# Kernel optimization log

Hardware: AMD Instinct MI355X
Metric: run time of the kernel (lower is better)

The kernel has to match this reference:

```python
import jax, jax.numpy as jnp
import numpy as np

G, S, P = 128, 32, 16          # graphs, subgraphs per graph, nodes per subgraph
D, C, NH, OUT = 768, 256, 4, 7 # input dim, hidden dim, GAT heads, classes


def setup_inputs() -> dict:
    key = jax.random.key(0)
    ks = jax.random.split(key, 17)
    n = lambda k, shape, s=0.05: jax.random.normal(k, shape, dtype=jnp.float32) * s
    return {
        "x": jax.random.normal(ks[0], (G, S, P, D), dtype=jnp.float32),
        # GATConv(768 -> 256, heads=4, concat=False): lin weight, att vectors, bias
        "gat_W": n(ks[1], (D, NH * C)),
        "att_src": n(ks[2], (NH, C)),
        "att_dst": n(ks[3], (NH, C)),
        "gat_b": n(ks[4], (C,)),
        # GRU(256 -> 256), torch layout [3*H, in]
        "gru_Wih": n(ks[5], (3 * C, C)),
        "gru_Whh": n(ks[6], (3 * C, C)),
        "gru_bih": n(ks[7], (3 * C,)),
        "gru_bhh": n(ks[8], (3 * C,)),
        # scale_up_projection Linear(256 -> 768)
        "up_W": n(ks[9], (D, C)),
        "up_b": n(ks[10], (D,)),
        # speaker_projection Linear(1536 -> 768) + ReLU
        "sp_W": n(ks[11], (D, 2 * D)),
        "sp_b": n(ks[12], (D,)),
        # GlobalAttention gate Linear(256 -> 1)
        "att_W": n(ks[13], (1, C)),
        "att_b": n(ks[14], (1,)),
        # classifier Linear(256 -> 7)
        "cls_W": n(ks[15], (OUT, C)),
        "cls_b": n(ks[16], (OUT,)),
    }


def _gat(x, W, a_src, a_dst, b):
    # PyG GATConv on a star graph (speaker = local node 0 -> all others) with
    # default add_self_loops=True, negative_slope=0.2, concat=False (mean over heads).
    # x: [G, P, D]
    h = jnp.einsum('gpd,dhc->gphc', x, W.reshape(D, NH, C))     # per-head transform
    es = jnp.sum(h * a_src, -1)                                 # [G, P, NH]
    ed = jnp.sum(h * a_dst, -1)
    lrelu = lambda v: jnp.where(v > 0, v, 0.2 * v)
    e_spk = lrelu(es[:, :1] + ed)   # edge speaker -> t
    e_slf = lrelu(es + ed)          # self loop t -> t
    w = jax.nn.softmax(jnp.stack([e_spk, e_slf], -1), axis=-1)  # [G, P, NH, 2]
    # for t == 0 both terms are h[:,0] and weights sum to 1, matching the
    # speaker node receiving only its self loop.
    out = w[..., 0:1] * h[:, :1] + w[..., 1:2] * h              # [G, P, NH, C]
    return out.mean(axis=2) + b


def _gru_cell(xin, h, Wih, Whh, bih, bhh):
    gi = xin @ Wih.T + bih
    gh = h @ Whh.T + bhh
    ir, iz, inn = jnp.split(gi, 3, -1)
    hr, hz, hn = jnp.split(gh, 3, -1)
    r = jax.nn.sigmoid(ir + hr)
    z = jax.nn.sigmoid(iz + hz)
    return (1 - z) * jnp.tanh(inn + r * hn) + z * h


def _forward(x, gat_W, att_src, att_dst, gat_b, gru_Wih, gru_Whh, gru_bih, gru_bhh,
             up_W, up_b, sp_W, sp_b, att_W, att_b, cls_W, cls_b):
    g, s, p, d = x.shape
    m0 = _gat(x[:, 0], gat_W, att_src, att_dst, gat_b)  # [G, P, C]
    h0 = jnp.zeros((g, p, C), x.dtype)

    def step(carry, _):
        h_run, m_prev = carry
        # running GRU hidden over memory prefix, then one zero-input step
        # (equivalent to rerunning the GRU over [m_0..m_{j-1}, 0])
        h_run = _gru_cell(m_prev, h_run, gru_Wih, gru_Whh, gru_bih, gru_bhh)
        h_nxt = _gru_cell(jnp.zeros_like(h_run), h_run, gru_Wih, gru_Whh, gru_bih, gru_bhh)
        pooled = h_nxt @ up_W.T + up_b                  # [G, P, D]
        # faithful to source: non_speaker_indices covers ALL nodes (torch.equal
        # shape-mismatch bug), and speaker_info is read AFTER the overwrite,
        # so the speaker concat is [pooled, pooled] and raw x[:, j>=1] is unused.
        spk = jnp.concatenate([pooled[:, 0], pooled[:, 0]], -1)  # [G, 2D]
        spk = jax.nn.relu(spk @ sp_W.T + sp_b)
        x_new = pooled.at[:, 0].set(spk)
        m = _gat(x_new, gat_W, att_src, att_dst, gat_b)
        return (h_run, m), m

    (_, _), ms = jax.lax.scan(step, (h0, m0), None, length=s - 1)
    mem = jnp.concatenate([m0[None], ms], axis=0)        # [S, G, P, C]
    # GlobalAttention pool over the P nodes of each subgraph memory state
    gate = jax.nn.softmax(jnp.squeeze(mem @ att_W.T + att_b, -1), axis=-1)  # [S, G, P]
    pooled = jnp.einsum('sgp,sgpc->sgc', gate, mem)
    logits = pooled @ cls_W.T + cls_b                    # [S, G, OUT]
    # torch stacks graph-major: [G*S, 1, OUT]
    return jnp.transpose(logits, (1, 0, 2)).reshape(g * s, 1, OUT)


def reference(x, gat_W, att_src, att_dst, gat_b, gru_Wih, gru_Whh, gru_bih, gru_bhh,
              up_W, up_b, sp_W, sp_b, att_W, att_b, cls_W, cls_b):
    return _forward(x, gat_W, att_src, att_dst, gat_b, gru_Wih, gru_Whh, gru_bih,
                    gru_bhh, up_W, up_b, sp_W, sp_b, att_W, att_b, cls_W, cls_b)
```

## Files before the change

kernel.cpp:

```cpp
#include <hip/hip_runtime.h>
#include <math.h>

#define NG 128
#define NS 32
#define NP 16
#define ND 768
#define NC 256
#define NHD 4
#define NOUT 7
#define NR 2048

typedef unsigned short ushortT;
typedef short bf16x8 __attribute__((ext_vector_type(8)));
typedef float f32x4 __attribute__((ext_vector_type(4)));

__device__ __forceinline__ ushortT f2b(float f) {
    union { float f; unsigned u; } v; v.f = f;
    unsigned r = (v.u + 0x7FFF + ((v.u >> 16) & 1)) >> 16;
    return (ushortT)r;
}
__device__ __forceinline__ float sigf(float v) { return 1.f / (1.f + expf(-v)); }

#define MFMA16(a, b, c) __builtin_amdgcn_mfma_f32_16x16x32_bf16((a), (b), (c), 0, 0, 0)

__global__ __launch_bounds__(256) void bgemm_kernel(
    const ushortT* __restrict__ A, const ushortT* __restrict__ Bt,
    const float* __restrict__ bias, float* __restrict__ outF,
    ushortT* __restrict__ outH, int N, int K, int act, int rowStride)
{
    __shared__ short As[64 * 40];
    __shared__ short Bs[64 * 40];
    const int tid = threadIdx.x;
    const int lane = tid & 63, wid = tid >> 6;
    const int quad = lane >> 4, l15 = lane & 15;
    const int row0 = blockIdx.y * 64, col0 = blockIdx.x * 64;
    const int mh = (wid & 1) * 32, nh = (wid >> 1) * 32;
    const int sr = tid >> 2, skq = (tid & 3) * 8;
    const ushortT* aptr = A + (size_t)(row0 + sr) * K;
    const ushortT* bptr = Bt + (size_t)(col0 + sr) * K;

    f32x4 acc[2][2];
    for (int i = 0; i < 2; ++i)
        for (int j = 0; j < 2; ++j) acc[i][j] = (f32x4){0.f, 0.f, 0.f, 0.f};

    for (int kk = 0; kk < K; kk += 32) {
        __syncthreads();
        *(uint4*)&As[sr * 40 + skq] = *(const uint4*)(aptr + kk + skq);
        *(uint4*)&Bs[sr * 40 + skq] = *(const uint4*)(bptr + kk + skq);
        __syncthreads();
        bf16x8 af0 = *(const bf16x8*)&As[(mh + l15) * 40 + quad * 8];
        bf16x8 af1 = *(const bf16x8*)&As[(mh + 16 + l15) * 40 + quad * 8];
        bf16x8 bf0 = *(const bf16x8*)&Bs[(nh + l15) * 40 + quad * 8];
        bf16x8 bf1 = *(const bf16x8*)&Bs[(nh + 16 + l15) * 40 + quad * 8];
        acc[0][0] = MFMA16(af0, bf0, acc[0][0]);
        acc[0][1] = MFMA16(af0, bf1, acc[0][1]);
        acc[1][0] = MFMA16(af1, bf0, acc[1][0]);
        acc[1][1] = MFMA16(af1, bf1, acc[1][1]);
    }
#pragma unroll
    for (int mt = 0; mt < 2; ++mt)
#pragma unroll
        for (int nt = 0; nt < 2; ++nt) {
            const int gc = col0 + nh + nt * 16 + l15;
            const float bv = bias ? bias[gc] : 0.f;
#pragma unroll
            for (int r = 0; r < 4; ++r) {
                const int gr = (row0 + mh + mt * 16 + quad * 4 + r) * rowStride;
                float v = acc[mt][nt][r] + bv;
                if (act) v = fmaxf(v, 0.f);
                if (outF) outF[(size_t)gr * N + gc] = v;
                if (outH) outH[(size_t)gr * N + gc] = f2b(v);
            }
        }
}

__global__ __launch_bounds__(256) void gru1_mfma_kernel(
    const ushortT* __restrict__ mB, const ushortT* __restrict__ hB,
    const ushortT* __restrict__ WihB, const ushortT* __restrict__ WhhB,
    const float* __restrict__ bih, const float* __restrict__ bhh,
    float* __restrict__ hF, ushortT* __restrict__ hBout)
{
    __shared__ short As[2 * 32 * 264];
    __shared__ short Bs[384 * 40];
    const int tid = threadIdx.x;
    const int lane = tid & 63, wid = tid >> 6;
    const int quad = lane >> 4, l15 = lane & 15;
    const int row0 = blockIdx.y * 32;
    const int n0 = blockIdx.x * 64;
    const int mt = wid & 1, nhh = (wid >> 1) * 32;

    for (int c = tid; c < 2048; c += 256) {
        const int mat = c >> 10, r2 = c & 1023, row = r2 >> 5, kc = (r2 & 31) * 8;
        const ushortT* src = (mat ? hB : mB) + (size_t)(row0 + row) * NC + kc;
        *(uint4*)&As[mat * 8448 + row * 264 + kc] = *(const uint4*)src;
    }
    f32x4 acc[2][3][2];
    for (int w = 0; w < 2; ++w)
        for (int g = 0; g < 3; ++g)
            for (int n = 0; n < 2; ++n) acc[w][g][n] = (f32x4){0.f, 0.f, 0.f, 0.f};

    for (int kk = 0; kk < 256; kk += 32) {
        __syncthreads();
        for (int c = tid; c < 1536; c += 256) {
            const int j = c >> 2, kq = (c & 3) * 8;
            const int w = j / 192, j2 = j - w * 192, gt = j2 >> 6, nloc = j2 & 63;
            const ushortT* src = (w ? WhhB : WihB) +
                (size_t)(gt * 256 + n0 + nloc) * NC + kk + kq;
            *(uint4*)&Bs[j * 40 + kq] = *(const uint4*)src;
        }
        __syncthreads();
        bf16x8 af0 = *(const bf16x8*)&As[(mt * 16 + l15) * 264 + kk + quad * 8];
        bf16x8 af1 = *(const bf16x8*)&As[8448 + (mt * 16 + l15) * 264 + kk + quad * 8];
#pragma unroll
        for (int gt = 0; gt < 3; ++gt)
#pragma unroll
            for (int nt = 0; nt < 2; ++nt) {
                const int jb = gt * 64 + nhh + nt * 16 + l15;
                bf16x8 b0 = *(const bf16x8*)&Bs[jb * 40 + quad * 8];
                bf16x8 b1 = *(const bf16x8*)&Bs[(192 + jb) * 40 + quad * 8];
                acc[0][gt][nt] = MFMA16(af0, b0, acc[0][gt][nt]);
                acc[1][gt][nt] = MFMA16(af1, b1, acc[1][gt][nt]);
            }
    }
#pragma unroll
    for (int nt = 0; nt < 2; ++nt) {
        const int c = n0 + nhh + nt * 16 + l15;
        const float br = bih[c], bz = bih[256 + c], bn = bih[512 + c];
        const float cr = bhh[c], cz = bhh[256 + c], cn = bhh[512 + c];
#pragma unroll
        for (int r = 0; r < 4; ++r) {
            const int grow = row0 + mt * 16 + quad * 4 + r;
            const size_t idx = (size_t)grow * NC + c;
            const float hold = hF[idx];
            const float rg = sigf(acc[0][0][nt][r] + br + acc[1][0][nt][r] + cr);
            const float zg = sigf(acc[0][1][nt][r] + bz + acc[1][1][nt][r] + cz);
            const float ng = tanhf(acc[0][2][nt][r] + bn + rg * (acc[1][2][nt][r] + cn));
            const float hn = (1.f - zg) * ng + zg * hold;
            hF[idx] = hn;
            hBout[idx] = f2b(hn);
        }
    }
}

__global__ __launch_bounds__(256) void gru2_mfma_kernel(
    const ushortT* __restrict__ hB, const ushortT* __restrict__ WhhB,
    const float* __restrict__ bih, const float* __restrict__ bhh,
    const float* __restrict__ hF, ushortT* __restrict__ hnB,
    ushortT* __restrict__ h0c)
{
    __shared__ short As[32 * 264];
    __shared__ short Bs[192 * 40];
    const int tid = threadIdx.x;
    const int lane = tid & 63, wid = tid >> 6;
    const int quad = lane >> 4, l15 = lane & 15;
    const int row0 = blockIdx.y * 32;
    const int n0 = blockIdx.x * 64;
    const int mt = wid & 1, nhh = (wid >> 1) * 32;

    for (int c = tid; c < 1024; c += 256) {
        const int row = c >> 5, kc = (c & 31) * 8;
        *(uint4*)&As[row * 264 + kc] =
            *(const uint4*)(hB + (size_t)(row0 + row) * NC + kc);
    }
    f32x4 acc[3][2];
    for (int g = 0; g < 3; ++g)
        for (int n = 0; n < 2; ++n) acc[g][n] = (f32x4){0.f, 0.f, 0.f, 0.f};

    for (int kk = 0; kk < 256; kk += 32) {
        __syncthreads();
        for (int c = tid; c < 768; c += 256) {
            const int j = c >> 2, kq = (c & 3) * 8;
            const int gt = j >> 6, nloc = j & 63;
            *(uint4*)&Bs[j * 40 + kq] =
                *(const uint4*)(WhhB + (size_t)(gt * 256 + n0 + nloc) * NC + kk + kq);
        }
        __syncthreads();
        bf16x8 af = *(const bf16x8*)&As[(mt * 16 + l15) * 264 + kk + quad * 8];
#pragma unroll
        for (int gt = 0; gt < 3; ++gt)
#pragma unroll
            for (int nt = 0; nt < 2; ++nt) {
                const int jb = gt * 64 + nhh + nt * 16 + l15;
                bf16x8 b = *(const bf16x8*)&Bs[jb * 40 + quad * 8];
                acc[gt][nt] = MFMA16(af, b, acc[gt][nt]);
            }
    }
#pragma unroll
    for (int nt = 0; nt < 2; ++nt) {
        const int c = n0 + nhh + nt * 16 + l15;
        const float br = bih[c], bz = bih[256 + c], bn = bih[512 + c];
        const float cr = bhh[c], cz = bhh[256 + c], cn = bhh[512 + c];
#pragma unroll
        for (int r = 0; r < 4; ++r) {
            const int grow = row0 + mt * 16 + quad * 4 + r;
            const size_t idx = (size_t)grow * NC + c;
            const float rg = sigf(br + acc[0][nt][r] + cr);
            const float zg = sigf(bz + acc[1][nt][r] + cz);
            const float ng = tanhf(bn + rg * (acc[2][nt][r] + cn));
            const float hv = (1.f - zg) * ng + zg * hF[idx];
            const ushortT hb = f2b(hv);
            hnB[idx] = hb;
            if ((grow & 15) == 0) h0c[(size_t)(grow >> 4) * NC + c] = hb;
        }
    }
}

__global__ __launch_bounds__(256) void fin_kernel(
    const float* __restrict__ hbuf, const float* __restrict__ att_src,
    const float* __restrict__ att_dst, const float* __restrict__ gat_b,
    const float* __restrict__ attW, const float* __restrict__ attb,
    const float* __restrict__ clsW, const float* __restrict__ clsb,
    ushortT* __restrict__ mB, float* __restrict__ outp, int s)
{
    const int g = blockIdx.x, tid = threadIdx.x;
    const int lane = tid & 63, wid = tid >> 6;
    __shared__ float es_s[16][4], ed_s[16][4];
    __shared__ float m_s[16][260];
    __shared__ float gate_s[16];
    __shared__ float pooled_s[256];
    const float* hb = hbuf + (size_t)g * NP * (NHD * NC);

    for (int pi = 0; pi < 4; ++pi) {
        const int p = wid * 4 + pi;
        const float* row = hb + p * (NHD * NC);
        float ss[4] = {0.f, 0.f, 0.f, 0.f}, sd[4] = {0.f, 0.f, 0.f, 0.f};
#pragma unroll
        for (int i = 0; i < 16; ++i) {
            const int col = lane + 64 * i;
            const float v = row[col];
            ss[i >> 2] += v * att_src[col];
            sd[i >> 2] += v * att_dst[col];
        }
        for (int off = 32; off; off >>= 1)
#pragma unroll
            for (int h = 0; h < 4; ++h) {
                ss[h] += __shfl_down(ss[h], off);
                sd[h] += __shfl_down(sd[h], off);
            }
        if (lane == 0)
#pragma unroll
            for (int h = 0; h < 4; ++h) { es_s[p][h] = ss[h]; ed_s[p][h] = sd[h]; }
    }
    __syncthreads();
    {
        const int p = tid >> 4, cb = (tid & 15) * 16;
        float accv[16];
#pragma unroll
        for (int cj = 0; cj < 16; ++cj) accv[cj] = 0.f;
#pragma unroll
        for (int h = 0; h < 4; ++h) {
            float e1 = es_s[0][h] + ed_s[p][h]; e1 = e1 > 0.f ? e1 : 0.2f * e1;
            float e2 = es_s[p][h] + ed_s[p][h]; e2 = e2 > 0.f ? e2 : 0.2f * e2;
            const float mx = fmaxf(e1, e2);
            float w0 = expf(e1 - mx), w1 = expf(e2 - mx);
            const float inv = 1.f / (w0 + w1);
            w0 *= inv; w1 *= inv;
            const float* r0 = hb + h * NC + cb;
            const float* rp = hb + p * (NHD * NC) + h * NC + cb;
#pragma unroll
            for (int cj = 0; cj < 16; ++cj) accv[cj] += w0 * r0[cj] + w1 * rp[cj];
        }
#pragma unroll
        for (int cj = 0; cj < 16; ++cj) {
            const float v = accv[cj] * 0.25f + gat_b[cb + cj];
            m_s[p][cb + cj] = v;
            mB[(size_t)(g * NP + p) * NC + cb + cj] = f2b(v);
        }
    }
    __syncthreads();
    for (int pi = 0; pi < 4; ++pi) {
        const int p = wid * 4 + pi;
        float sg = 0.f;
#pragma unroll
        for (int i = 0; i < 4; ++i) { const int c = lane + 64 * i; sg += m_s[p][c] * attW[c]; }
        for (int off = 32; off; off >>= 1) sg += __shfl_down(sg, off);
        if (lane == 0) gate_s[p] = sg + attb[0];
    }
    __syncthreads();
    float mx = -1e30f;
#pragma unroll
    for (int p = 0; p < 16; ++p) mx = fmaxf(mx, gate_s[p]);
    float ge[16], ssum = 0.f;
#pragma unroll
    for (int p = 0; p < 16; ++p) { ge[p] = expf(gate_s[p] - mx); ssum += ge[p]; }
    const float inv = 1.f / ssum;
    {
        float pc = 0.f;
#pragma unroll
        for (int p = 0; p < 16; ++p) pc += ge[p] * m_s[p][tid];
        pooled_s[tid] = pc * inv;
    }
    __syncthreads();
    const int o = tid >> 5, l32 = tid & 31;
    if (o < NOUT) {
        float a = 0.f;
#pragma unroll
        for (int i = 0; i < 8; ++i) {
            const int c = l32 + 32 * i;
            a += pooled_s[c] * clsW[o * NC + c];
        }
        for (int off = 16; off; off >>= 1) a += __shfl_down(a, off);
        if (l32 == 0) outp[((size_t)g * NS + s) * NOUT + o] = a + clsb[o];
    }
}

__global__ __launch_bounds__(256) void cast_kernel(const float* __restrict__ a,
                                                   ushortT* __restrict__ b, int n) {
    const int i = blockIdx.x * 256 + threadIdx.x;
    if (i < n) b[i] = f2b(a[i]);
}
__global__ __launch_bounds__(256) void gatT_kernel(const float* __restrict__ gW,
                                                   ushortT* __restrict__ gB) {
    const int idx = blockIdx.x * 256 + threadIdx.x;
    const int c = idx / ND, d = idx - c * ND;
    gB[idx] = f2b(gW[(size_t)d * (NHD * NC) + c]);
}
__global__ __launch_bounds__(256) void upwT_kernel(const float* __restrict__ upW,
                                                   ushortT* __restrict__ o) {
    const int idx = blockIdx.x * 256 + threadIdx.x;
    const int k = idx / ND, d = idx - k * ND;
    o[idx] = f2b(upW[(size_t)d * NC + k]);
}
__global__ __launch_bounds__(256) void bcomb_kernel(const float* __restrict__ gW,
                                                    const float* __restrict__ up_b,
                                                    float* __restrict__ bc) {
    const int c = blockIdx.x * 256 + threadIdx.x;
    if (c >= NHD * NC) return;
    float a = 0.f;
    for (int d = 0; d < ND; ++d) a += up_b[d] * gW[(size_t)d * (NHD * NC) + c];
    bc[c] = a;
}
__global__ __launch_bounds__(256) void spwc_kernel(const float* __restrict__ spW,
                                                   float* __restrict__ o) {
    const int idx = blockIdx.x * 256 + threadIdx.x;
    const int r = idx / ND, d = idx - r * ND;
    o[idx] = spW[(size_t)r * (2 * ND) + d] + spW[(size_t)r * (2 * ND) + ND + d];
}
__global__ __launch_bounds__(256) void wus_kernel(const float* __restrict__ spWc,
                                                  const float* __restrict__ upW,
                                                  ushortT* __restrict__ WusB) {
    const int c = threadIdx.x;
    const int o0 = blockIdx.x * 16;
    float acc[16];
#pragma unroll
    for (int i = 0; i < 16; ++i) acc[i] = 0.f;
    for (int d = 0; d < ND; ++d) {
        const float u = upW[(size_t)d * NC + c];
#pragma unroll
        for (int i = 0; i < 16; ++i) acc[i] += spWc[(size_t)(o0 + i) * ND + d] * u;
    }
#pragma unroll
    for (int i = 0; i < 16; ++i) WusB[(size_t)(o0 + i) * NC + c] = f2b(acc[i]);
}
__global__ __launch_bounds__(256) void bus_kernel(const float* __restrict__ spWc,
                                                  const float* __restrict__ up_b,
                                                  const float* __restrict__ sp_b,
                                                  float* __restrict__ bus) {
    const int o = blockIdx.x * 256 + threadIdx.x;
    if (o >= ND) return;
    float a = sp_b[o];
    const float* sr = spWc + (size_t)o * ND;
    for (int d = 0; d < ND; ++d) a += sr[d] * up_b[d];
    bus[o] = a;
}
__global__ __launch_bounds__(256) void x0_kernel(const float* __restrict__ x,
                                                 ushortT* __restrict__ xb) {
    const int idx = blockIdx.x * 256 + threadIdx.x;
    const int row = idx / ND, d = idx - row * ND;
    const int g = row >> 4, p = row & 15;
    xb[idx] = f2b(x[((size_t)g * (NS * NP) + p) * ND + d]);
}
__global__ __launch_bounds__(256) void zh_kernel(float* hF, ushortT* hB) {
    const int idx = blockIdx.x * 256 + threadIdx.x;
    hF[idx] = 0.f;
    hB[idx] = 0;
}

extern "C" void kernel_launch(void* const* d_in, const int* in_sizes, int n_in,
                              void* d_out, int out_size, void* d_ws, size_t ws_size,
                              hipStream_t stream) {
    (void)in_sizes; (void)n_in; (void)out_size; (void)ws_size;
    const float* x       = (const float*)d_in[0];
    const float* gat_W   = (const float*)d_in[1];
    const float* att_src = (const float*)d_in[2];
    const float* att_dst = (const float*)d_in[3];
    const float* gat_b   = (const float*)d_in[4];
    const float* gru_Wih = (const float*)d_in[5];
    const float* gru_Whh = (const float*)d_in[6];
    const float* gru_bih = (const float*)d_in[7];
    const float* gru_bhh = (const float*)d_in[8];
    const float* up_W    = (const float*)d_in[9];
    const float* up_b    = (const float*)d_in[10];
    const float* sp_W    = (const float*)d_in[11];
    const float* sp_b    = (const float*)d_in[12];
    const float* att_W   = (const float*)d_in[13];
    const float* att_b   = (const float*)d_in[14];
    const float* cls_W   = (const float*)d_in[15];
    const float* cls_b   = (const float*)d_in[16];
    float* outp = (float*)d_out;

    char* w = (char*)d_ws;
    ushortT* xb    = (ushortT*)w; w += (size_t)NR * ND * 2;
    ushortT* WihB  = (ushortT*)w; w += (size_t)(3 * NC) * NC * 2;
    ushortT* WhhB  = (ushortT*)w; w += (size_t)(3 * NC) * NC * 2;
    ushortT* gatB  = (ushortT*)w; w += (size_t)(NHD * NC) * ND * 2;
    ushortT* WusB  = (ushortT*)w; w += (size_t)ND * NC * 2;
    ushortT* upWT  = (ushortT*)w; w += (size_t)NC * ND * 2;
    ushortT* WcombB= (ushortT*)w; w += (size_t)(NHD * NC) * NC * 2;
    float*   bcomb = (float*)w;   w += (size_t)(NHD * NC) * 4;
    float*   spWc  = (float*)w;   w += (size_t)ND * ND * 4;
    float*   bus   = (float*)w;   w += (size_t)ND * 4;
    float*   hF    = (float*)w;   w += (size_t)NR * NC * 4;
    ushortT* hB    = (ushortT*)w; w += (size_t)NR * NC * 2;
    ushortT* hnB   = (ushortT*)w; w += (size_t)NR * NC * 2;
    ushortT* h0c   = (ushortT*)w; w += (size_t)NG * NC * 2;
    ushortT* spkB  = (ushortT*)w; w += (size_t)NG * ND * 2;
    float*   hbuf  = (float*)w;   w += (size_t)NR * (NHD * NC) * 4;
    ushortT* mB    = (ushortT*)w; w += (size_t)NR * NC * 2;

    cast_kernel<<<768, 256, 0, stream>>>(gru_Wih, WihB, 3 * NC * NC);
    cast_kernel<<<768, 256, 0, stream>>>(gru_Whh, WhhB, 3 * NC * NC);
    gatT_kernel<<<(NHD * NC * ND) / 256, 256, 0, stream>>>(gat_W, gatB);
    upwT_kernel<<<(NC * ND) / 256, 256, 0, stream>>>(up_W, upWT);
    bcomb_kernel<<<(NHD * NC) / 256, 256, 0, stream>>>(gat_W, up_b, bcomb);
    spwc_kernel<<<(ND * ND) / 256, 256, 0, stream>>>(sp_W, spWc);
    wus_kernel<<<ND / 16, 256, 0, stream>>>(spWc, up_W, WusB);
    bus_kernel<<<3, 256, 0, stream>>>(spWc, up_b, sp_b, bus);
    x0_kernel<<<(NR * ND) / 256, 256, 0, stream>>>(x, xb);
    zh_kernel<<<(NR * NC) / 256, 256, 0, stream>>>(hF, hB);
    bgemm_kernel<<<dim3(NC / 64, (NHD * NC) / 64), 256, 0, stream>>>(
        gatB, upWT, nullptr, nullptr, WcombB, NC, ND, 0, 1);

    bgemm_kernel<<<dim3((NHD * NC) / 64, NR / 64), 256, 0, stream>>>(
        xb, gatB, nullptr, hbuf, nullptr, NHD * NC, ND, 0, 1);
    fin_kernel<<<NG, 256, 0, stream>>>(hbuf, att_src, att_dst, gat_b,
                                       att_W, att_b, cls_W, cls_b, mB, outp, 0);

    for (int j = 1; j < NS; ++j) {
        gru1_mfma_kernel<<<dim3(NC / 64, NR / 32), 256, 0, stream>>>(
            mB, hB, WihB, WhhB, gru_bih, gru_bhh, hF, hB);
        gru2_mfma_kernel<<<dim3(NC / 64, NR / 32), 256, 0, stream>>>(
            hB, WhhB, gru_bih, gru_bhh, hF, hnB, h0c);
        bgemm_kernel<<<dim3(ND / 64, NG / 64), 256, 0, stream>>>(
            h0c, WusB, bus, nullptr, spkB, ND, NC, 1, 1);
        bgemm_kernel<<<dim3((NHD * NC) / 64, NR / 64), 256, 0, stream>>>(
            hnB, WcombB, bcomb, hbuf, nullptr, NHD * NC, NC, 0, 1);
        bgemm_kernel<<<dim3((NHD * NC) / 64, NG / 64), 256, 0, stream>>>(
            spkB, gatB, nullptr, hbuf, nullptr, NHD * NC, ND, 0, 16);
        fin_kernel<<<NG, 256, 0, stream>>>(hbuf, att_src, att_dst, gat_b,
                                           att_W, att_b, cls_W, cls_b, mB, outp, j);
    }
}
```

Baseline: 2.630 ms.

## Fuse entire recurrent GRU/GAT time loop into one persistent per-graph kernel

Replaces the per-timestep sequence of GRU, projection, GAT GEMM and finalize kernel launches with a single kernel that runs one block per graph across all timesteps. Hidden state, GAT features and memory stay in shared memory and registers instead of round-tripping through global buffers, and the input cast and zero-init kernels are folded in. This removes launch overhead and global traffic. The cost is only 128 blocks of parallelism, and every block streams the weights from global/L2 without LDS tiling at each step.

```diff
diff --git a/kernel.cpp b/kernel.cpp
--- a/kernel.cpp
+++ b/kernel.cpp
@@ -19,14 +19,306 @@
     unsigned r = (v.u + 0x7FFF + ((v.u >> 16) & 1)) >> 16;
     return (ushortT)r;
 }
+__device__ __forceinline__ float b2f(ushortT u) {
+    union { unsigned u; float f; } v; v.u = ((unsigned)u) << 16; return v.f;
+}
 __device__ __forceinline__ float sigf(float v) { return 1.f / (1.f + expf(-v)); }
 
 #define MFMA16(a, b, c) __builtin_amdgcn_mfma_f32_16x16x32_bf16((a), (b), (c), 0, 0, 0)
+
+__global__ __launch_bounds__(512, 2) void mega_kernel(
+    const float* __restrict__ x,
+    const ushortT* __restrict__ WihB, const ushortT* __restrict__ WhhB,
+    const ushortT* __restrict__ WcombB, const float* __restrict__ bcomb,
+    const ushortT* __restrict__ gatB, const ushortT* __restrict__ WusB,
+    const float* __restrict__ busv,
+    const float* __restrict__ bih, const float* __restrict__ bhh,
+    const float* __restrict__ att_src, const float* __restrict__ att_dst,
+    const float* __restrict__ gat_b, const float* __restrict__ attW,
+    const float* __restrict__ attb, const float* __restrict__ clsW,
+    const float* __restrict__ clsb, float* __restrict__ outp)
+{
+    __shared__ float hb[16][1032];
+    __shared__ float m_f[16][264];
+    __shared__ ushortT hrun_b[16][264];
+    __shared__ ushortT hnxt_b[16][264];
+    __shared__ ushortT spk_b[800];
+    __shared__ float ats_s[1024], atd_s[1024], gatb_s[256];
+    __shared__ float es_s[16][4], ed_s[16][4], gate_s[16], pooled_s[256];
+
+    const int g = blockIdx.x, tid = threadIdx.x;
+    const int w = tid >> 6, lane = tid & 63;
+    const int quad = lane >> 4, l15 = lane & 15;
+
+    for (int i = tid; i < 1024; i += 512) { ats_s[i] = att_src[i]; atd_s[i] = att_dst[i]; }
+    for (int i = tid; i < 256; i += 512) gatb_s[i] = gat_b[i];
+    for (int i = tid; i < 16 * 264; i += 512) ((ushortT*)hrun_b)[i] = 0;
+    float hreg[2][4];
+#pragma unroll
+    for (int nt = 0; nt < 2; ++nt)
+#pragma unroll
+        for (int r = 0; r < 4; ++r) hreg[nt][r] = 0.f;
+    __syncthreads();
+
+    auto fin = [&](int s) {
+        for (int p = w; p < 16; p += 8) {
+            const float* row = hb[p];
+            float ss[4] = {0.f, 0.f, 0.f, 0.f}, sd[4] = {0.f, 0.f, 0.f, 0.f};
+#pragma unroll
+            for (int i = 0; i < 16; ++i) {
+                const int col = lane + 64 * i;
+                const float v = row[col];
+                ss[i >> 2] += v * ats_s[col];
+                sd[i >> 2] += v * atd_s[col];
+            }
+            for (int off = 32; off; off >>= 1)
+#pragma unroll
+                for (int h = 0; h < 4; ++h) {
+                    ss[h] += __shfl_down(ss[h], off);
+                    sd[h] += __shfl_down(sd[h], off);
+                }
+            if (lane == 0)
+#pragma unroll
+                for (int h = 0; h < 4; ++h) { es_s[p][h] = ss[h]; ed_s[p][h] = sd[h]; }
+        }
+        __syncthreads();
+        {
+            const int p = tid >> 5, cb = (tid & 31) * 8;
+            float accv[8];
+#pragma unroll
+            for (int cj = 0; cj < 8; ++cj) accv[cj] = 0.f;
+#pragma unroll
+            for (int h = 0; h < 4; ++h) {
+                float e1 = es_s[0][h] + ed_s[p][h]; e1 = e1 > 0.f ? e1 : 0.2f * e1;
+                float e2 = es_s[p][h] + ed_s[p][h]; e2 = e2 > 0.f ? e2 : 0.2f * e2;
+                const float mx = fmaxf(e1, e2);
+                float w0 = expf(e1 - mx), w1 = expf(e2 - mx);
+                const float inv = 1.f / (w0 + w1);
+                w0 *= inv; w1 *= inv;
+                const float* r0 = &hb[0][h * NC + cb];
+                const float* rp = &hb[p][h * NC + cb];
+#pragma unroll
+                for (int cj = 0; cj < 8; ++cj) accv[cj] += w0 * r0[cj] + w1 * rp[cj];
+            }
+#pragma unroll
+            for (int cj = 0; cj < 8; ++cj)
+                m_f[p][cb + cj] = accv[cj] * 0.25f + gatb_s[cb + cj];
+        }
+        __syncthreads();
+        for (int p = w; p < 16; p += 8) {
+            float sg = 0.f;
+#pragma unroll
+            for (int i = 0; i < 4; ++i) { const int c = lane + 64 * i; sg += m_f[p][c] * attW[c]; }
+            for (int off = 32; off; off >>= 1) sg += __shfl_down(sg, off);
+            if (lane == 0) gate_s[p] = sg + attb[0];
+        }
+        __syncthreads();
+        if (tid < 256) {
+            float mx = -1e30f;
+#pragma unroll
+            for (int p = 0; p < 16; ++p) mx = fmaxf(mx, gate_s[p]);
+            float se = 0.f, pc = 0.f;
+#pragma unroll
+            for (int p = 0; p < 16; ++p) {
+                const float e = expf(gate_s[p] - mx);
+                se += e; pc += e * m_f[p][tid];
+            }
+            pooled_s[tid] = pc / se;
+        }
+        __syncthreads();
+        if (w < NOUT) {
+            float a = 0.f;
+#pragma unroll
+            for (int i = 0; i < 4; ++i) {
+                const int c = lane + 64 * i;
+                a += pooled_s[c] * clsW[w * NC + c];
+            }
+            for (int off = 32; off; off >>= 1) a += __shfl_down(a, off);
+            if (lane == 0) outp[((size_t)g * NS + s) * NOUT + w] = a + clsb[w];
+        }
+        __syncthreads();
+    };
+
+    {
+        const float* xg = x + (size_t)g * (NS * NP * ND);
+        f32x4 a0[8];
+#pragma unroll
+        for (int t = 0; t < 8; ++t) a0[t] = (f32x4){0.f, 0.f, 0.f, 0.f};
+        for (int kk = 0; kk < ND; kk += 32) {
+            const float* ap = xg + (size_t)l15 * ND + kk + quad * 8;
+            bf16x8 af;
+#pragma unroll
+            for (int i = 0; i < 8; ++i) af[i] = (short)f2b(ap[i]);
+#pragma unroll
+            for (int t = 0; t < 8; ++t) {
+                const int col = w * 128 + t * 16 + l15;
+                bf16x8 bv = *(const bf16x8*)(gatB + (size_t)col * ND + kk + quad * 8);
+                a0[t] = MFMA16(af, bv, a0[t]);
+            }
+        }
+#pragma unroll
+        for (int t = 0; t < 8; ++t) {
+            const int col = w * 128 + t * 16 + l15;
+#pragma unroll
+            for (int r = 0; r < 4; ++r) hb[quad * 4 + r][col] = a0[t][r];
+        }
+    }
+    __syncthreads();
+    fin(0);
+
+    for (int j = 1; j < NS; ++j) {
+        {
+            f32x4 a1[2][3][2];
+#pragma unroll
+            for (int mm = 0; mm < 2; ++mm)
+#pragma unroll
+                for (int gt = 0; gt < 3; ++gt)
+#pragma unroll
+                    for (int nt = 0; nt < 2; ++nt) a1[mm][gt][nt] = (f32x4){0.f, 0.f, 0.f, 0.f};
+            for (int kk = 0; kk < NC; kk += 32) {
+                const float* mp = &m_f[l15][kk + quad * 8];
+                bf16x8 afm;
+#pragma unroll
+                for (int i = 0; i < 8; ++i) afm[i] = (short)f2b(mp[i]);
+                bf16x8 afh = *(const bf16x8*)&hrun_b[l15][kk + quad * 8];
+#pragma unroll
+                for (int gt = 0; gt < 3; ++gt)
+#pragma unroll
+                    for (int nt = 0; nt < 2; ++nt) {
+                        const int col = gt * 256 + w * 32 + nt * 16 + l15;
+                        bf16x8 b1 = *(const bf16x8*)(WihB + (size_t)col * NC + kk + quad * 8);
+                        bf16x8 b2 = *(const bf16x8*)(WhhB + (size_t)col * NC + kk + quad * 8);
+                        a1[0][gt][nt] = MFMA16(afm, b1, a1[0][gt][nt]);
+                        a1[1][gt][nt] = MFMA16(afh, b2, a1[1][gt][nt]);
+                    }
+            }
+            __syncthreads();
+#pragma unroll
+            for (int nt = 0; nt < 2; ++nt) {
+                const int c = w * 32 + nt * 16 + l15;
+                const float br = bih[c], bz = bih[256 + c], bn = bih[512 + c];
+                const float cr = bhh[c], cz = bhh[256 + c], cn = bhh[512 + c];
+#pragma unroll
+                for (int r = 0; r < 4; ++r) {
+                    const int row = quad * 4 + r;
+                    const float rg = sigf(a1[0][0][nt][r] + br + a1[1][0][nt][r] + cr);
+                    const float zg = sigf(a1[0][1][nt][r] + bz + a1[1][1][nt][r] + cz);
+                    const float ng = tanhf(a1[0][2][nt][r] + bn + rg * (a1[1][2][nt][r] + cn));
+                    const float hn = (1.f - zg) * ng + zg * hreg[nt][r];
+                    hreg[nt][r] = hn;
+                    hrun_b[row][c] = f2b(hn);
+                }
+            }
+        }
+        __syncthreads();
+
+        {
+            f32x4 a2[3][2];
+#pragma unroll
+            for (int gt = 0; gt < 3; ++gt)
+#pragma unroll
+                for (int nt = 0; nt < 2; ++nt) a2[gt][nt] = (f32x4){0.f, 0.f, 0.f, 0.f};
+            for (int kk = 0; kk < NC; kk += 32) {
+                bf16x8 afh = *(const bf16x8*)&hrun_b[l15][kk + quad * 8];
+#pragma unroll
+                for (int gt = 0; gt < 3; ++gt)
+#pragma unroll
+                    for (int nt = 0; nt < 2; ++nt) {
+                        const int col = gt * 256 + w * 32 + nt * 16 + l15;
+                        bf16x8 b2 = *(const bf16x8*)(WhhB + (size_t)col * NC + kk + quad * 8);
+                        a2[gt][nt] = MFMA16(afh, b2, a2[gt][nt]);
+                    }
+            }
+#pragma unroll
+            for (int nt = 0; nt < 2; ++nt) {
+                const int c = w * 32 + nt * 16 + l15;
+                const float br = bih[c], bz = bih[256 + c], bn = bih[512 + c];
+                const float cr = bhh[c], cz = bhh[256 + c], cn = bhh[512 + c];
+#pragma unroll
+                for (int r = 0; r < 4; ++r) {
+                    const int row = quad * 4 + r;
+                    const float rg = sigf(br + a2[0][nt][r] + cr);
+                    const float zg = sigf(bz + a2[1][nt][r] + cz);
+                    const float ng = tanhf(bn + rg * (a2[2][nt][r] + cn));
+                    const float hv = (1.f - zg) * ng + zg * hreg[nt][r];
+                    hnxt_b[row][c] = f2b(hv);
+                }
+            }
+        }
+        __syncthreads();
+
+        for (int it = 0; it < 6; ++it) {
+            const int slot = it * 512 + tid;
+            const int o = slot >> 2, part = slot & 3;
+            float s = 0.f;
+#pragma unroll
+            for (int k8 = 0; k8 < 8; ++k8) {
+                const int k = part * 64 + k8 * 8;
+                bf16x8 hv8 = *(const bf16x8*)&hnxt_b[0][k];
+                bf16x8 wv8 = *(const bf16x8*)(WusB + (size_t)o * NC + k);
+#pragma unroll
+                for (int i = 0; i < 8; ++i) s += b2f((ushortT)hv8[i]) * b2f((ushortT)wv8[i]);
+            }
+            s += __shfl_down(s, 1);
+            s += __shfl_down(s, 2);
+            if (part == 0) spk_b[o] = f2b(fmaxf(s + busv[o], 0.f));
+        }
+        __syncthreads();
+
+        {
+            f32x4 ag[8];
+#pragma unroll
+            for (int t = 0; t < 8; ++t) ag[t] = (f32x4){0.f, 0.f, 0.f, 0.f};
+            for (int kk = 0; kk < NC; kk += 32) {
+                bf16x8 af;
+                if (l15 == 0) {
+#pragma unroll
+                    for (int i = 0; i < 8; ++i) af[i] = 0;
+                } else {
+                    af = *(const bf16x8*)&hnxt_b[l15][kk + quad * 8];
+                }
+#pragma unroll
+                for (int t = 0; t < 8; ++t) {
+                    const int col = w * 128 + t * 16 + l15;
+                    bf16x8 bv = *(const bf16x8*)(WcombB + (size_t)col * NC + kk + quad * 8);
+                    ag[t] = MFMA16(af, bv, ag[t]);
+                }
+            }
+            for (int kk = 0; kk < ND; kk += 32) {
+                bf16x8 af;
+                if (l15 == 0) {
+                    af = *(const bf16x8*)&spk_b[kk + quad * 8];
+                } else {
+#pragma unroll
+                    for (int i = 0; i < 8; ++i) af[i] = 0;
+                }
+#pragma unroll
+                for (int t = 0; t < 8; ++t) {
+                    const int col = w * 128 + t * 16 + l15;
+                    bf16x8 bv = *(const bf16x8*)(gatB + (size_t)col * ND + kk + quad * 8);
+                    ag[t] = MFMA16(af, bv, ag[t]);
+                }
+            }
+#pragma unroll
+            for (int t = 0; t < 8; ++t) {
+                const int col = w * 128 + t * 16 + l15;
+                const float bc = bcomb[col];
+#pragma unroll
+                for (int r = 0; r < 4; ++r) {
+                    const int row = quad * 4 + r;
+                    hb[row][col] = ag[t][r] + (row ? bc : 0.f);
+                }
+            }
+        }
+        __syncthreads();
+
+        fin(j);
+    }
+}
 
 __global__ __launch_bounds__(256) void bgemm_kernel(
     const ushortT* __restrict__ A, const ushortT* __restrict__ Bt,
-    const float* __restrict__ bias, float* __restrict__ outF,
-    ushortT* __restrict__ outH, int N, int K, int act, int rowStride)
+    ushortT* __restrict__ outH, int N, int K)
 {
     __shared__ short As[64 * 40];
     __shared__ short Bs[64 * 40];
@@ -62,246 +354,12 @@
 #pragma unroll
         for (int nt = 0; nt < 2; ++nt) {
             const int gc = col0 + nh + nt * 16 + l15;
-            const float bv = bias ? bias[gc] : 0.f;
 #pragma unroll
             for (int r = 0; r < 4; ++r) {
-                const int gr = (row0 + mh + mt * 16 + quad * 4 + r) * rowStride;
-                float v = acc[mt][nt][r] + bv;
-                if (act) v = fmaxf(v, 0.f);
-                if (outF) outF[(size_t)gr * N + gc] = v;
-                if (outH) outH[(size_t)gr * N + gc] = f2b(v);
-            }
-        }
-}
-
-__global__ __launch_bounds__(256) void gru1_mfma_kernel(
-    const ushortT* __restrict__ mB, const ushortT* __restrict__ hB,
-    const ushortT* __restrict__ WihB, const ushortT* __restrict__ WhhB,
-    const float* __restrict__ bih, const float* __restrict__ bhh,
-    float* __restrict__ hF, ushortT* __restrict__ hBout)
-{
-    __shared__ short As[2 * 32 * 264];
-    __shared__ short Bs[384 * 40];
-    const int tid = threadIdx.x;
-    const int lane = tid & 63, wid = tid >> 6;
-    const int quad = lane >> 4, l15 = lane & 15;
-    const int row0 = blockIdx.y * 32;
-    const int n0 = blockIdx.x * 64;
-    const int mt = wid & 1, nhh = (wid >> 1) * 32;
-
-    for (int c = tid; c < 2048; c += 256) {
-        const int mat = c >> 10, r2 = c & 1023, row = r2 >> 5, kc = (r2 & 31) * 8;
-        const ushortT* src = (mat ? hB : mB) + (size_t)(row0 + row) * NC + kc;
-        *(uint4*)&As[mat * 8448 + row * 264 + kc] = *(const uint4*)src;
-    }
-    f32x4 acc[2][3][2];
-    for (int w = 0; w < 2; ++w)
-        for (int g = 0; g < 3; ++g)
-            for (int n = 0; n < 2; ++n) acc[w][g][n] = (f32x4){0.f, 0.f, 0.f, 0.f};
-
-    for (int kk = 0; kk < 256; kk += 32) {
-        __syncthreads();
-        for (int c = tid; c < 1536; c += 256) {
-            const int j = c >> 2, kq = (c & 3) * 8;
-            const int w = j / 192, j2 = j - w * 192, gt = j2 >> 6, nloc = j2 & 63;
-            const ushortT* src = (w ? WhhB : WihB) +
-                (size_t)(gt * 256 + n0 + nloc) * NC + kk + kq;
-            *(uint4*)&Bs[j * 40 + kq] = *(const uint4*)src;
-        }
-        __syncthreads();
-        bf16x8 af0 = *(const bf16x8*)&As[(mt * 16 + l15) * 264 + kk + quad * 8];
-        bf16x8 af1 = *(const bf16x8*)&As[8448 + (mt * 16 + l15) * 264 + kk + quad * 8];
-#pragma unroll
-        for (int gt = 0; gt < 3; ++gt)
-#pragma unroll
-            for (int nt = 0; nt < 2; ++nt) {
-                const int jb = gt * 64 + nhh + nt * 16 + l15;
-                bf16x8 b0 = *(const bf16x8*)&Bs[jb * 40 + quad * 8];
-                bf16x8 b1 = *(const bf16x8*)&Bs[(192 + jb) * 40 + quad * 8];
-                acc[0][gt][nt] = MFMA16(af0, b0, acc[0][gt][nt]);
-                acc[1][gt][nt] = MFMA16(af1, b1, acc[1][gt][nt]);
-            }
-    }
-#pragma unroll
-    for (int nt = 0; nt < 2; ++nt) {
-        const int c = n0 + nhh + nt * 16 + l15;
-        const float br = bih[c], bz = bih[256 + c], bn = bih[512 + c];
-        const float cr = bhh[c], cz = bhh[256 + c], cn = bhh[512 + c];
-#pragma unroll
-        for (int r = 0; r < 4; ++r) {
-            const int grow = row0 + mt * 16 + quad * 4 + r;
-            const size_t idx = (size_t)grow * NC + c;
-            const float hold = hF[idx];
-            const float rg = sigf(acc[0][0][nt][r] + br + acc[1][0][nt][r] + cr);
-            const float zg = sigf(acc[0][1][nt][r] + bz + acc[1][1][nt][r] + cz);
-            const float ng = tanhf(acc[0][2][nt][r] + bn + rg * (acc[1][2][nt][r] + cn));
-            const float hn = (1.f - zg) * ng + zg * hold;
-            hF[idx] = hn;
-            hBout[idx] = f2b(hn);
-        }
-    }
-}
-
-__global__ __launch_bounds__(256) void gru2_mfma_kernel(
-    const ushortT* __restrict__ hB, const ushortT* __restrict__ WhhB,
-    const float* __restrict__ bih, const float* __restrict__ bhh,
-    const float* __restrict__ hF, ushortT* __restrict__ hnB,
-    ushortT* __restrict__ h0c)
-{
-    __shared__ short As[32 * 264];
-    __shared__ short Bs[192 * 40];
-    const int tid = threadIdx.x;
-    const int lane = tid & 63, wid = tid >> 6;
-    const int quad = lane >> 4, l15 = lane & 15;
-    const int row0 = blockIdx.y * 32;
-    const int n0 = blockIdx.x * 64;
-    const int mt = wid & 1, nhh = (wid >> 1) * 32;
-
-    for (int c = tid; c < 1024; c += 256) {
-        const int row = c >> 5, kc = (c & 31) * 8;
-        *(uint4*)&As[row * 264 + kc] =
-            *(const uint4*)(hB + (size_t)(row0 + row) * NC + kc);
-    }
-    f32x4 acc[3][2];
-    for (int g = 0; g < 3; ++g)
-        for (int n = 0; n < 2; ++n) acc[g][n] = (f32x4){0.f, 0.f, 0.f, 0.f};
-
-    for (int kk = 0; kk < 256; kk += 32) {
-        __syncthreads();
-        for (int c = tid; c < 768; c += 256) {
-            const int j = c >> 2, kq = (c & 3) * 8;
-            const int gt = j >> 6, nloc = j & 63;
-            *(uint4*)&Bs[j * 40 + kq] =
-                *(const uint4*)(WhhB + (size_t)(gt * 256 + n0 + nloc) * NC + kk + kq);
-        }
-        __syncthreads();
-        bf16x8 af = *(const bf16x8*)&As[(mt * 16 + l15) * 264 + kk + quad * 8];
-#pragma unroll
-        for (int gt = 0; gt < 3; ++gt)
-#pragma unroll
-            for (int nt = 0; nt < 2; ++nt) {
-                const int jb = gt * 64 + nhh + nt * 16 + l15;
-                bf16x8 b = *(const bf16x8*)&Bs[jb * 40 + quad * 8];
-                acc[gt][nt] = MFMA16(af, b, acc[gt][nt]);
-            }
-    }
-#pragma unroll
-    for (int nt = 0; nt < 2; ++nt) {
-        const int c = n0 + nhh + nt * 16 + l15;
-        const float br = bih[c], bz = bih[256 + c], bn = bih[512 + c];
-        const float cr = bhh[c], cz = bhh[256 + c], cn = bhh[512 + c];
-#pragma unroll
-        for (int r = 0; r < 4; ++r) {
-            const int grow = row0 + mt * 16 + quad * 4 + r;
-            const size_t idx = (size_t)grow * NC + c;
-            const float rg = sigf(br + acc[0][nt][r] + cr);
-            const float zg = sigf(bz + acc[1][nt][r] + cz);
-            const float ng = tanhf(bn + rg * (acc[2][nt][r] + cn));
-            const float hv = (1.f - zg) * ng + zg * hF[idx];
-            const ushortT hb = f2b(hv);
-            hnB[idx] = hb;
-            if ((grow & 15) == 0) h0c[(size_t)(grow >> 4) * NC + c] = hb;
-        }
-    }
-}
-
-__global__ __launch_bounds__(256) void fin_kernel(
-    const float* __restrict__ hbuf, const float* __restrict__ att_src,
-    const float* __restrict__ att_dst, const float* __restrict__ gat_b,
-    const float* __restrict__ attW, const float* __restrict__ attb,
-    const float* __restrict__ clsW, const float* __restrict__ clsb,
-    ushortT* __restrict__ mB, float* __restrict__ outp, int s)
-{
-    const int g = blockIdx.x, tid = threadIdx.x;
-    const int lane = tid & 63, wid = tid >> 6;
-    __shared__ float es_s[16][4], ed_s[16][4];
-    __shared__ float m_s[16][260];
-    __shared__ float gate_s[16];
-    __shared__ float pooled_s[256];
-    const float* hb = hbuf + (size_t)g * NP * (NHD * NC);
-
-    for (int pi = 0; pi < 4; ++pi) {
-        const int p = wid * 4 + pi;
-        const float* row = hb + p * (NHD * NC);
-        float ss[4] = {0.f, 0.f, 0.f, 0.f}, sd[4] = {0.f, 0.f, 0.f, 0.f};
-#pragma unroll
-        for (int i = 0; i < 16; ++i) {
-            const int col = lane + 64 * i;
-            const float v = row[col];
-            ss[i >> 2] += v * att_src[col];
-            sd[i >> 2] += v * att_dst[col];
-        }
-        for (int off = 32; off; off >>= 1)
-#pragma unroll
-            for (int h = 0; h < 4; ++h) {
-                ss[h] += __shfl_down(ss[h], off);
-                sd[h] += __shfl_down(sd[h], off);
-            }
-        if (lane == 0)
-#pragma unroll
-            for (int h = 0; h < 4; ++h) { es_s[p][h] = ss[h]; ed_s[p][h] = sd[h]; }
-    }
-    __syncthreads();
-    {
-        const int p = tid >> 4, cb = (tid & 15) * 16;
-        float accv[16];
-#pragma unroll
-        for (int cj = 0; cj < 16; ++cj) accv[cj] = 0.f;
-#pragma unroll
-        for (int h = 0; h < 4; ++h) {
-            float e1 = es_s[0][h] + ed_s[p][h]; e1 = e1 > 0.f ? e1 : 0.2f * e1;
-            float e2 = es_s[p][h] + ed_s[p][h]; e2 = e2 > 0.f ? e2 : 0.2f * e2;
-            const float mx = fmaxf(e1, e2);
-            float w0 = expf(e1 - mx), w1 = expf(e2 - mx);
-            const float inv = 1.f / (w0 + w1);
-            w0 *= inv; w1 *= inv;
-            const float* r0 = hb + h * NC + cb;
-            const float* rp = hb + p * (NHD * NC) + h * NC + cb;
-#pragma unroll
-            for (int cj = 0; cj < 16; ++cj) accv[cj] += w0 * r0[cj] + w1 * rp[cj];
-        }
-#pragma unroll
-        for (int cj = 0; cj < 16; ++cj) {
-            const float v = accv[cj] * 0.25f + gat_b[cb + cj];
-            m_s[p][cb + cj] = v;
-            mB[(size_t)(g * NP + p) * NC + cb + cj] = f2b(v);
-        }
-    }
-    __syncthreads();
-    for (int pi = 0; pi < 4; ++pi) {
-        const int p = wid * 4 + pi;
-        float sg = 0.f;
-#pragma unroll
-        for (int i = 0; i < 4; ++i) { const int c = lane + 64 * i; sg += m_s[p][c] * attW[c]; }
-        for (int off = 32; off; off >>= 1) sg += __shfl_down(sg, off);
-        if (lane == 0) gate_s[p] = sg + attb[0];
-    }
-    __syncthreads();
-    float mx = -1e30f;
-#pragma unroll
-    for (int p = 0; p < 16; ++p) mx = fmaxf(mx, gate_s[p]);
-    float ge[16], ssum = 0.f;
-#pragma unroll
-    for (int p = 0; p < 16; ++p) { ge[p] = expf(gate_s[p] - mx); ssum += ge[p]; }
-    const float inv = 1.f / ssum;
-    {
-        float pc = 0.f;
-#pragma unroll
-        for (int p = 0; p < 16; ++p) pc += ge[p] * m_s[p][tid];
-        pooled_s[tid] = pc * inv;
-    }
-    __syncthreads();
-    const int o = tid >> 5, l32 = tid & 31;
-    if (o < NOUT) {
-        float a = 0.f;
-#pragma unroll
-        for (int i = 0; i < 8; ++i) {
-            const int c = l32 + 32 * i;
-            a += pooled_s[c] * clsW[o * NC + c];
-        }
-        for (int off = 16; off; off >>= 1) a += __shfl_down(a, off);
-        if (l32 == 0) outp[((size_t)g * NS + s) * NOUT + o] = a + clsb[o];
-    }
+                const int gr = row0 + mh + mt * 16 + quad * 4 + r;
+                outH[(size_t)gr * N + gc] = f2b(acc[mt][nt][r]);
+            }
+        }
 }
 
 __global__ __launch_bounds__(256) void cast_kernel(const float* __restrict__ a,
@@ -362,18 +420,6 @@
     const float* sr = spWc + (size_t)o * ND;
     for (int d = 0; d < ND; ++d) a += sr[d] * up_b[d];
     bus[o] = a;
-}
-__global__ __launch_bounds__(256) void x0_kernel(const float* __restrict__ x,
-                                                 ushortT* __restrict__ xb) {
-    const int idx = blockIdx.x * 256 + threadIdx.x;
-    const int row = idx / ND, d = idx - row * ND;
-    const int g = row >> 4, p = row & 15;
-    xb[idx] = f2b(x[((size_t)g * (NS * NP) + p) * ND + d]);
-}
-__global__ __launch_bounds__(256) void zh_kernel(float* hF, ushortT* hB) {
-    const int idx = blockIdx.x * 256 + threadIdx.x;
-    hF[idx] = 0.f;
-    hB[idx] = 0;
 }
 
 extern "C" void kernel_launch(void* const* d_in, const int* in_sizes, int n_in,
@@ -400,23 +446,15 @@
     float* outp = (float*)d_out;
 
     char* w = (char*)d_ws;
-    ushortT* xb    = (ushortT*)w; w += (size_t)NR * ND * 2;
     ushortT* WihB  = (ushortT*)w; w += (size_t)(3 * NC) * NC * 2;
     ushortT* WhhB  = (ushortT*)w; w += (size_t)(3 * NC) * NC * 2;
     ushortT* gatB  = (ushortT*)w; w += (size_t)(NHD * NC) * ND * 2;
-    ushortT* WusB  = (ushortT*)w; w += (size_t)ND * NC * 2;
     ushortT* upWT  = (ushortT*)w; w += (size_t)NC * ND * 2;
     ushortT* WcombB= (ushortT*)w; w += (size_t)(NHD * NC) * NC * 2;
+    ushortT* WusB  = (ushortT*)w; w += (size_t)ND * NC * 2;
     float*   bcomb = (float*)w;   w += (size_t)(NHD * NC) * 4;
     float*   spWc  = (float*)w;   w += (size_t)ND * ND * 4;
     float*   bus   = (float*)w;   w += (size_t)ND * 4;
-    float*   hF    = (float*)w;   w += (size_t)NR * NC * 4;
-    ushortT* hB    = (ushortT*)w; w += (size_t)NR * NC * 2;
-    ushortT* hnB   = (ushortT*)w; w += (size_t)NR * NC * 2;
-    ushortT* h0c   = (ushortT*)w; w += (size_t)NG * NC * 2;
-    ushortT* spkB  = (ushortT*)w; w += (size_t)NG * ND * 2;
-    float*   hbuf  = (float*)w;   w += (size_t)NR * (NHD * NC) * 4;
-    ushortT* mB    = (ushortT*)w; w += (size_t)NR * NC * 2;
 
     cast_kernel<<<768, 256, 0, stream>>>(gru_Wih, WihB, 3 * NC * NC);
     cast_kernel<<<768, 256, 0, stream>>>(gru_Whh, WhhB, 3 * NC * NC);
@@ -426,28 +464,11 @@
     spwc_kernel<<<(ND * ND) / 256, 256, 0, stream>>>(sp_W, spWc);
     wus_kernel<<<ND / 16, 256, 0, stream>>>(spWc, up_W, WusB);
     bus_kernel<<<3, 256, 0, stream>>>(spWc, up_b, sp_b, bus);
-    x0_kernel<<<(NR * ND) / 256, 256, 0, stream>>>(x, xb);
-    zh_kernel<<<(NR * NC) / 256, 256, 0, stream>>>(hF, hB);
     bgemm_kernel<<<dim3(NC / 64, (NHD * NC) / 64), 256, 0, stream>>>(
-        gatB, upWT, nullptr, nullptr, WcombB, NC, ND, 0, 1);
-
-    bgemm_kernel<<<dim3((NHD * NC) / 64, NR / 64), 256, 0, stream>>>(
-        xb, gatB, nullptr, hbuf, nullptr, NHD * NC, ND, 0, 1);
-    fin_kernel<<<NG, 256, 0, stream>>>(hbuf, att_src, att_dst, gat_b,
-                                       att_W, att_b, cls_W, cls_b, mB, outp, 0);
-
-    for (int j = 1; j < NS; ++j) {
-        gru1_mfma_kernel<<<dim3(NC / 64, NR / 32), 256, 0, stream>>>(
-            mB, hB, WihB, WhhB, gru_bih, gru_bhh, hF, hB);
-        gru2_mfma_kernel<<<dim3(NC / 64, NR / 32), 256, 0, stream>>>(
-            hB, WhhB, gru_bih, gru_bhh, hF, hnB, h0c);
-        bgemm_kernel<<<dim3(ND / 64, NG / 64), 256, 0, stream>>>(
-            h0c, WusB, bus, nullptr, spkB, ND, NC, 1, 1);
-        bgemm_kernel<<<dim3((NHD * NC) / 64, NR / 64), 256, 0, stream>>>(
-            hnB, WcombB, bcomb, hbuf, nullptr, NHD * NC, NC, 0, 1);
-        bgemm_kernel<<<dim3((NHD * NC) / 64, NG / 64), 256, 0, stream>>>(
-            spkB, gatB, nullptr, hbuf, nullptr, NHD * NC, ND, 0, 16);
-        fin_kernel<<<NG, 256, 0, stream>>>(hbuf, att_src, att_dst, gat_b,
-                                           att_W, att_b, cls_W, cls_b, mB, outp, j);
-    }
-}
+        gatB, upWT, WcombB, NC, ND);
+
+    mega_kernel<<<NG, 512, 0, stream>>>(
+        x, WihB, WhhB, WcombB, bcomb, gatB, WusB, bus,
+        gru_bih, gru_bhh, att_src, att_dst, gat_b,
+        att_W, att_b, cls_W, cls_b, outp);
+}
```

New measurement: 6.765 ms. +157.2%, slower.
